# Performance work log

Hardware: AMD Instinct MI355X
Metric: run time of the kernel (lower is better)

Reference implementation:

```python
import jax, jax.numpy as jnp
import numpy as np
import math

B_, L_, E_, N_, K_, R_ = 2, 4096, 2048, 16, 4, 64


def setup_inputs() -> dict:
    key = jax.random.key(0)
    ks = jax.random.split(key, 8)
    x_inner = jax.random.normal(ks[0], (B_, L_, E_), jnp.float32)
    # depthwise conv params (weight squeezed to (E, K))
    conv_w = jax.random.normal(ks[1], (E_, K_), jnp.float32) * (1.0 / math.sqrt(K_))
    conv_b = jax.random.normal(ks[2], (E_,), jnp.float32) * 0.02
    # x_proj: Linear(E -> R + 2N), no bias; weight stored (out, in)
    x_proj_w = jax.random.normal(ks[3], (R_ + 2 * N_, E_), jnp.float32) * (E_ ** -0.5)
    # dt_proj: Linear(R -> E) with Mamba dt init
    dt_proj_w = jax.random.uniform(ks[4], (E_, R_), jnp.float32, -(E_ ** -0.5), E_ ** -0.5)
    dt = jnp.exp(jax.random.uniform(ks[5], (E_,), jnp.float32) * (math.log(0.1) - math.log(0.001)) + math.log(0.001))
    dt = jnp.clip(dt, 1e-4, None)
    dt_proj_b = dt + jnp.log(-jnp.expm1(-dt))  # inverse softplus
    # A_log: log of arange(1..N) tiled over channels; D = ones
    A_log = jnp.log(jnp.tile(jnp.arange(1, N_ + 1, dtype=jnp.float32), (E_, 1)))
    D = jnp.ones((E_,), jnp.float32)
    return {"x_inner": x_inner, "conv_w": conv_w, "conv_b": conv_b,
            "x_proj_w": x_proj_w, "dt_proj_w": dt_proj_w, "dt_proj_b": dt_proj_b,
            "A_log": A_log, "D": D}


def _forward(x_inner, conv_w, conv_b, x_proj_w, dt_proj_w, dt_proj_b, A_log, D):
    B, L, E = x_inner.shape
    N = A_log.shape[1]
    K = conv_w.shape[1]
    R = dt_proj_w.shape[1]
    # ---- causal depthwise conv1d + SiLU ----
    x_t = jnp.transpose(x_inner, (0, 2, 1))  # (B, E, L)
    x_t = jax.lax.conv_general_dilated(
        x_t, conv_w[:, None, :],  # (O=E, I=1, K)
        window_strides=(1,), padding=[(K - 1, 0)],
        feature_group_count=E,
        dimension_numbers=("NCH", "OIH", "NCH")) + conv_b[None, :, None]
    x_conv = jax.nn.silu(jnp.transpose(x_t, (0, 2, 1)))  # (B, L, E)
    # ---- input-dependent SSM parameters ----
    x_dbl = jnp.einsum("ble,oe->blo", x_conv, x_proj_w)  # (B, L, R+2N)
    dt_lowrank = x_dbl[..., :R]
    Bm = x_dbl[..., R:R + N]       # (B, L, N)
    Cm = x_dbl[..., R + N:]        # (B, L, N)
    delta = jax.nn.softplus(jnp.einsum("blr,er->ble", dt_lowrank, dt_proj_w) + dt_proj_b)  # (B, L, E)
    A = -jnp.exp(A_log)            # (E, N)
    # ---- selective scan over sequence ----
    def step(h, inp):
        d_t, b_t, c_t, u_t = inp   # (B,E), (B,N), (B,N), (B,E)
        dA = jnp.exp(d_t[..., None] * A)              # (B, E, N)
        h = dA * h + (d_t * u_t)[..., None] * b_t[:, None, :]
        y_t = jnp.einsum("ben,bn->be", h, c_t)
        return h, y_t

    h0 = jnp.zeros((B, E, N), x_conv.dtype)
    xs = (jnp.transpose(delta, (1, 0, 2)), jnp.transpose(Bm, (1, 0, 2)),
          jnp.transpose(Cm, (1, 0, 2)), jnp.transpose(x_conv, (1, 0, 2)))
    _, ys = jax.lax.scan(step, h0, xs)
    y = jnp.transpose(ys, (1, 0, 2)) + x_conv * D  # skip term D*u
    return y  # (B, L, E)


def reference(x_inner, conv_w, conv_b, x_proj_w, dt_proj_w, dt_proj_b, A_log, D):
    return _forward(x_inner, conv_w, conv_b, x_proj_w, dt_proj_w, dt_proj_b, A_log, D)
```

## Files before the change

### kernel.cpp

```cpp
#include <hip/hip_runtime.h>
#include <cstdint>
#include <cstddef>

#define BB 2
#define LL 4096
#define EE 2048
#define NN 16
#define RR 64
#define NCH 64
#define LC  64
#define BL  (BB*LL)
#define KS  16
#define STRIP 16

static constexpr size_t OFF_XCONV = 0;
static constexpr size_t OFF_DELTA = OFF_XCONV + (size_t)BB*LL*EE;
static constexpr size_t OFF_XDT   = OFF_DELTA + (size_t)BB*LL*EE;
static constexpr size_t OFF_P     = OFF_XDT   + (size_t)96*BL;
static constexpr size_t OFF_S     = OFF_P     + (size_t)NCH*BB*NN*EE;
static constexpr size_t OFF_H0    = OFF_S     + (size_t)NCH*BB*NN*EE;
static constexpr size_t OFF_BC    = OFF_H0    + (size_t)NCH*BB*NN*EE;
static constexpr size_t OFF_PART  = OFF_P;

#define L2E 1.4426950408889634f

__device__ __forceinline__ float fast_softplus(float z) {
  if (z > 20.f) return z;
  return 0.6931471805599453f * __log2f(1.f + __builtin_amdgcn_exp2f(z * L2E));
}

__global__ __launch_bounds__(256) void k_conv(const float* __restrict__ x,
    const float* __restrict__ cw, const float* __restrict__ cb,
    float* __restrict__ xc) {
  const int t     = threadIdx.x;
  const int eh    = blockIdx.x & 1;
  const int strip = (blockIdx.x >> 1) & (LL/STRIP - 1);
  const int b     = blockIdx.x >> 9;
  const int e0    = (eh*256 + t) * 4;
  const int l0    = strip * STRIP;
  const float4* cw4 = (const float4*)cw;
  const float4 w0 = cw4[e0 + 0], w1 = cw4[e0 + 1], w2 = cw4[e0 + 2], w3 = cw4[e0 + 3];
  const float b0 = cb[e0 + 0], b1 = cb[e0 + 1], b2 = cb[e0 + 2], b3 = cb[e0 + 3];
  const float* base = x + (size_t)b*LL*EE + e0;
  float* obase = xc + (size_t)b*LL*EE + e0;
  float4 win0, win1, win2;
  {
    const float4 z = make_float4(0.f, 0.f, 0.f, 0.f);
    win0 = (l0 - 3 >= 0) ? *(const float4*)(base + (size_t)(l0-3)*EE) : z;
    win1 = (l0 - 2 >= 0) ? *(const float4*)(base + (size_t)(l0-2)*EE) : z;
    win2 = (l0 - 1 >= 0) ? *(const float4*)(base + (size_t)(l0-1)*EE) : z;
  }
  #pragma unroll
  for (int i = 0; i < STRIP; ++i) {
    const int l = l0 + i;
    const float4 cur = *(const float4*)(base + (size_t)l*EE);
    float a0 = b0 + win0.x*w0.x + win1.x*w0.y + win2.x*w0.z + cur.x*w0.w;
    float a1 = b1 + win0.y*w1.x + win1.y*w1.y + win2.y*w1.z + cur.y*w1.w;
    float a2 = b2 + win0.z*w2.x + win1.z*w2.y + win2.z*w2.z + cur.z*w2.w;
    float a3 = b3 + win0.w*w3.x + win1.w*w3.y + win2.w*w3.z + cur.w*w3.w;
    a0 = a0 / (1.f + __builtin_amdgcn_exp2f(-a0 * L2E));
    a1 = a1 / (1.f + __builtin_amdgcn_exp2f(-a1 * L2E));
    a2 = a2 / (1.f + __builtin_amdgcn_exp2f(-a2 * L2E));
    a3 = a3 / (1.f + __builtin_amdgcn_exp2f(-a3 * L2E));
    float4 o; o.x = a0; o.y = a1; o.z = a2; o.w = a3;
    *(float4*)(obase + (size_t)l*EE) = o;
    win0 = win1; win1 = win2; win2 = cur;
  }
}

__global__ __launch_bounds__(256, 2) void k_xdbl(const float* __restrict__ xc,
    const float* __restrict__ xpw, float* __restrict__ part) {
  __shared__ float xs[128*36];
  __shared__ float wsh[96*34];
  const int t  = threadIdx.x;
  const int mt = blockIdx.x >> 4;
  const int ks = blockIdx.x & 15;
  const int row0  = mt * 128;
  const int kbase = ks * (EE/KS);
  const int tr = t & 15;
  const int tc = t >> 4;
  const int c0 = 6 * tc;
  float acc[8][6];
  #pragma unroll
  for (int i = 0; i < 8; ++i)
    #pragma unroll
    for (int j = 0; j < 6; ++j) acc[i][j] = 0.f;

  const int xr = t >> 3;
  const int xk = (t & 7) * 4;
  const int wo = t >> 5;
  const int wk = t & 31;

  for (int ch = 0; ch < (EE/KS)/32; ++ch) {
    const int koff = kbase + ch * 32;
    __syncthreads();
    #pragma unroll
    for (int p = 0; p < 4; ++p) {
      int r = xr + 32 * p;
      float4 v = *(const float4*)(xc + (size_t)(row0 + r)*EE + koff + xk);
      *(float4*)(xs + r*36 + xk) = v;
    }
    #pragma unroll
    for (int p = 0; p < 12; ++p) {
      int o = wo + 8 * p;
      wsh[o*34 + wk] = xpw[(size_t)o*EE + koff + wk];
    }
    __syncthreads();
    #pragma unroll
    for (int kk = 0; kk < 32; kk += 2) {
      float2 xf[8], wf[6];
      #pragma unroll
      for (int i = 0; i < 8; ++i) xf[i] = *(const float2*)(xs + (tr + 16*i)*36 + kk);
      #pragma unroll
      for (int j = 0; j < 6; ++j) wf[j] = *(const float2*)(wsh + (c0 + j)*34 + kk);
      #pragma unroll
      for (int i = 0; i < 8; ++i)
        #pragma unroll
        for (int j = 0; j < 6; ++j) {
          acc[i][j] += xf[i].x * wf[j].x;
          acc[i][j] += xf[i].y * wf[j].y;
        }
    }
  }
  #pragma unroll
  for (int i = 0; i < 8; ++i)
    #pragma unroll
    for (int j = 0; j < 6; ++j)
      part[((size_t)ks*96 + (c0 + j))*BL + row0 + tr + 16*i] = acc[i][j];
}

__global__ __launch_bounds__(256) void k_combine(const float* __restrict__ part,
    float* __restrict__ xdT) {
  int i = blockIdx.x * 256 + threadIdx.x;
  float4 s = ((const float4*)part)[i];
  #pragma unroll
  for (int ks = 1; ks < KS; ++ks) {
    float4 v = ((const float4*)part)[(size_t)ks*(96*BL/4) + i];
    s.x += v.x; s.y += v.y; s.z += v.z; s.w += v.w;
  }
  ((float4*)xdT)[i] = s;
}

__global__ __launch_bounds__(256) void k_pack(const float* __restrict__ xdT,
    float* __restrict__ BC) {
  __shared__ float tile[64][33];
  const int t = threadIdx.x;
  const int bl0 = blockIdx.x * 64;
  const int jr = t >> 6, bll = t & 63;
  #pragma unroll
  for (int p = 0; p < 8; ++p) {
    int j = jr + 4 * p;
    tile[bll][j] = xdT[(size_t)(64 + j)*BL + bl0 + bll];
  }
  __syncthreads();
  const int blw = t >> 3;
  const int j4 = (t & 7) * 4;
  #pragma unroll
  for (int p = 0; p < 2; ++p) {
    int bl = blw + 32 * p;
    float4 v = make_float4(tile[bl][j4], tile[bl][j4+1], tile[bl][j4+2], tile[bl][j4+3]);
    *(float4*)(BC + (size_t)(bl0 + bl)*32 + j4) = v;
  }
}

__global__ __launch_bounds__(256, 2) void k_delta(const float* __restrict__ xdT,
    const float* __restrict__ dtw, const float* __restrict__ dtb,
    float* __restrict__ dl) {
  __shared__ float xs[128*66];
  __shared__ float wsh[128*66];
  const int t  = threadIdx.x;
  const int rt = blockIdx.x >> 4;
  const int et = blockIdx.x & 15;
  const int row0 = rt * 128;
  const int eb   = et * 128;
  #pragma unroll
  for (int p = 0; p < 32; ++p) {
    int idx = t + 256*p;
    int k = idx >> 7, rr = idx & 127;
    xs[rr*66 + k] = xdT[(size_t)k*BL + row0 + rr];
  }
  #pragma unroll
  for (int p = 0; p < 32; ++p) {
    int idx = t + 256*p;
    int e = idx >> 6, k = idx & 63;
    wsh[e*66 + k] = dtw[(size_t)(eb + e)*RR + k];
  }
  __syncthreads();
  const int tr = t >> 4;
  const int tc = t & 15;
  float acc[8][8];
  #pragma unroll
  for (int i = 0; i < 8; ++i)
    #pragma unroll
    for (int j = 0; j < 8; ++j) acc[i][j] = 0.f;
  for (int k = 0; k < 64; k += 2) {
    float2 xf[8], wf[8];
    #pragma unroll
    for (int i = 0; i < 8; ++i) xf[i] = *(const float2*)(xs + (tr + 16*i)*66 + k);
    #pragma unroll
    for (int j = 0; j < 8; ++j) wf[j] = *(const float2*)(wsh + (tc + 16*j)*66 + k);
    #pragma unroll
    for (int i = 0; i < 8; ++i)
      #pragma unroll
      for (int j = 0; j < 8; ++j) {
        acc[i][j] += xf[i].x * wf[j].x;
        acc[i][j] += xf[i].y * wf[j].y;
      }
  }
  #pragma unroll
  for (int j = 0; j < 8; ++j) {
    int e = eb + tc + 16*j;
    float bias = dtb[e];
    #pragma unroll
    for (int i = 0; i < 8; ++i) {
      float z = acc[i][j] + bias;
      dl[(size_t)(row0 + tr + 16*i)*EE + e] = fast_softplus(z);
    }
  }
}

__global__ __launch_bounds__(256) void k_scanA(const float* __restrict__ dl,
    const float* __restrict__ xc, const float* __restrict__ BC,
    float* __restrict__ P, float* __restrict__ S) {
  const int t  = threadIdx.x;
  const int eb = (blockIdx.x & 7) << 8;
  const int b  = (blockIdx.x >> 3) & 1;
  const int c  = blockIdx.x >> 4;
  const int e  = eb + t;
  const int l0 = c * LC;
  float h[NN];
  #pragma unroll
  for (int n = 0; n < NN; ++n) h[n] = 0.f;
  const float* dp = dl + (size_t)(b*LL + l0)*EE + e;
  const float* up = xc + (size_t)(b*LL + l0)*EE + e;
  const float* bc = BC + (size_t)(b*LL + l0)*32;
  float dsum = 0.f;
  float d_nx = dp[0], u_nx = up[0];
  #pragma unroll 2
  for (int l = 0; l < LC; ++l) {
    float d = d_nx, u = u_nx;
    d_nx = dp[(size_t)(l+1)*EE];
    u_nx = up[(size_t)(l+1)*EE];
    float w = d * u;
    dsum += d;
    float q = __builtin_amdgcn_exp2f(-d * L2E);
    float pw[NN];
    pw[0]=q; pw[1]=q*q; pw[2]=pw[1]*q; pw[3]=pw[1]*pw[1];
    pw[4]=pw[3]*q; pw[5]=pw[3]*pw[1]; pw[6]=pw[3]*pw[2]; pw[7]=pw[3]*pw[3];
    #pragma unroll
    for (int n = 8; n < 16; ++n) pw[n] = pw[7]*pw[n-8];
    #pragma unroll
    for (int n = 0; n < NN; ++n)
      h[n] = pw[n]*h[n] + w*bc[l*32 + n];
  }
  float Q = __builtin_amdgcn_exp2f(-dsum * L2E);
  float Pq[NN];
  Pq[0]=Q; Pq[1]=Q*Q; Pq[2]=Pq[1]*Q; Pq[3]=Pq[1]*Pq[1];
  Pq[4]=Pq[3]*Q; Pq[5]=Pq[3]*Pq[1]; Pq[6]=Pq[3]*Pq[2]; Pq[7]=Pq[3]*Pq[3];
  #pragma unroll
  for (int n = 8; n < 16; ++n) Pq[n] = Pq[7]*Pq[n-8];
  const size_t base = (size_t)(c*BB + b)*NN*EE + e;
  #pragma unroll
  for (int n = 0; n < NN; ++n) { P[base + (size_t)n*EE] = Pq[n]; S[base + (size_t)n*EE] = h[n]; }
}

__global__ __launch_bounds__(256) void k_chain(const float* __restrict__ P,
    const float* __restrict__ S, float* __restrict__ h0) {
  int i = blockIdx.x * 256 + threadIdx.x;
  float h = 0.f;
  float Pc = P[i], Sc = S[i];
  for (int c = 0; c < NCH; ++c) {
    size_t idx = (size_t)c*(BB*NN*EE) + i;
    float Pn = 0.f, Sn = 0.f;
    if (c + 1 < NCH) {
      Pn = P[idx + (size_t)(BB*NN*EE)];
      Sn = S[idx + (size_t)(BB*NN*EE)];
    }
    h0[idx] = h;
    h = Pc*h + Sc;
    Pc = Pn; Sc = Sn;
  }
}

__global__ __launch_bounds__(256) void k_scanY(const float* __restrict__ dl,
    const float* __restrict__ xc, const float* __restrict__ BC,
    const float* __restrict__ h0, const float* __restrict__ Dp,
    float* __restrict__ out) {
  const int t  = threadIdx.x;
  const int eb = (blockIdx.x & 7) << 8;
  const int b  = (blockIdx.x >> 3) & 1;
  const int c  = blockIdx.x >> 4;
  const int e  = eb + t;
  const int l0 = c * LC;
  float h[NN];
  #pragma unroll
  for (int n = 0; n < NN; ++n)
    h[n] = h0[(size_t)c*(BB*NN*EE) + (size_t)b*(NN*EE) + (size_t)n*EE + e];
  const float Dv = Dp[e];
  const float* dp = dl + (size_t)(b*LL + l0)*EE + e;
  const float* up = xc + (size_t)(b*LL + l0)*EE + e;
  const float* bc = BC + (size_t)(b*LL + l0)*32;
  float* op = out + (size_t)(b*LL + l0)*EE + e;
  float d_nx = dp[0], u_nx = up[0];
  #pragma unroll 2
  for (int l = 0; l < LC; ++l) {
    float d = d_nx, u = u_nx;
    d_nx = dp[(size_t)(l+1)*EE];
    u_nx = up[(size_t)(l+1)*EE];
    float w = d * u;
    float q = __builtin_amdgcn_exp2f(-d * L2E);
    float pw[NN];
    pw[0]=q; pw[1]=q*q; pw[2]=pw[1]*q; pw[3]=pw[1]*pw[1];
    pw[4]=pw[3]*q; pw[5]=pw[3]*pw[1]; pw[6]=pw[3]*pw[2]; pw[7]=pw[3]*pw[3];
    #pragma unroll
    for (int n = 8; n < 16; ++n) pw[n] = pw[7]*pw[n-8];
    float y0 = 0.f, y1 = 0.f, y2 = 0.f, y3 = 0.f;
    #pragma unroll
    for (int n = 0; n < NN; ++n) {
      h[n] = pw[n]*h[n] + w*bc[l*32 + n];
      float hv = h[n] * bc[l*32 + 16 + n];
      if ((n & 3) == 0) y0 += hv; else if ((n & 3) == 1) y1 += hv;
      else if ((n & 3) == 2) y2 += hv; else y3 += hv;
    }
    op[(size_t)l*EE] = (y0 + y1) + (y2 + y3) + u*Dv;
  }
}

extern "C" void kernel_launch(void* const* d_in, const int* in_sizes, int n_in,
                              void* d_out, int out_size, void* d_ws, size_t ws_size,
                              hipStream_t stream) {
  const float* x    = (const float*)d_in[0];
  const float* cw   = (const float*)d_in[1];
  const float* cb   = (const float*)d_in[2];
  const float* xpw  = (const float*)d_in[3];
  const float* dtw  = (const float*)d_in[4];
  const float* dtb  = (const float*)d_in[5];
  const float* Dp   = (const float*)d_in[7];
  float* ws = (float*)d_ws;
  float* xconv = ws + OFF_XCONV;
  float* delta = ws + OFF_DELTA;
  float* xdT   = ws + OFF_XDT;
  float* part  = ws + OFF_PART;
  float* P     = ws + OFF_P;
  float* S     = ws + OFF_S;
  float* h0    = ws + OFF_H0;
  float* BC    = ws + OFF_BC;
  float* out   = (float*)d_out;

  k_conv   <<<BB*2*(LL/STRIP),    256, 0, stream>>>(x, cw, cb, xconv);
  k_xdbl   <<<64*KS,              256, 0, stream>>>(xconv, xpw, part);
  k_combine<<<(96*BL/4)/256,      256, 0, stream>>>(part, xdT);
  k_pack   <<<BL/64,              256, 0, stream>>>(xdT, BC);
  k_delta  <<<64*16,              256, 0, stream>>>(xdT, dtw, dtb, delta);
  k_scanA  <<<(EE/256)*BB*NCH,    256, 0, stream>>>(delta, xconv, BC, P, S);
  k_chain  <<<(BB*NN*EE)/256,     256, 0, stream>>>(P, S, h0);
  k_scanY  <<<(EE/256)*BB*NCH,    256, 0, stream>>>(delta, xconv, BC, h0, Dp, out);
}
```

Before: 330.0 us.

## Use split-bf16 MFMA for x_proj GEMM and store conv output as bf16 hi/lo

The x_proj GEMM moves from scalar FP32 FMAs to bf16 MFMA 16x16x32 instructions. Each FP32 value is split into a bf16 high part and a bf16 low residual, and three MFMAs per tile recover near-FP32 accuracy. The conv kernel now writes x_conv as two bf16 planes, and a new kernel converts the weights the same way. The scans rebuild u from both planes, and the K-split drops from 16 to 4, so the partial sums and the combine step shrink. The truncating conversion and the dropped lo*lo term cost some precision, and the scans do extra unpacking work.

```diff
diff --git a/kernel.cpp b/kernel.cpp
--- a/kernel.cpp
+++ b/kernel.cpp
@@ -10,49 +10,74 @@
 #define NCH 64
 #define LC  64
 #define BL  (BB*LL)
-#define KS  16
+#define KSX 4
+#define AKS (EE/KSX)
 #define STRIP 16
 
-static constexpr size_t OFF_XCONV = 0;
-static constexpr size_t OFF_DELTA = OFF_XCONV + (size_t)BB*LL*EE;
+static constexpr size_t OFF_XCH   = 0;
+static constexpr size_t OFF_XCL   = OFF_XCH + (size_t)BB*LL*EE/2;
+static constexpr size_t OFF_DELTA = OFF_XCL + (size_t)BB*LL*EE/2;
 static constexpr size_t OFF_XDT   = OFF_DELTA + (size_t)BB*LL*EE;
 static constexpr size_t OFF_P     = OFF_XDT   + (size_t)96*BL;
 static constexpr size_t OFF_S     = OFF_P     + (size_t)NCH*BB*NN*EE;
 static constexpr size_t OFF_H0    = OFF_S     + (size_t)NCH*BB*NN*EE;
 static constexpr size_t OFF_BC    = OFF_H0    + (size_t)NCH*BB*NN*EE;
 static constexpr size_t OFF_PART  = OFF_P;
+static constexpr size_t OFF_WHL   = OFF_S;
 
 #define L2E 1.4426950408889634f
+
+typedef __attribute__((ext_vector_type(8))) short short8;
+typedef __attribute__((ext_vector_type(4))) float f32x4;
 
 __device__ __forceinline__ float fast_softplus(float z) {
   if (z > 20.f) return z;
   return 0.6931471805599453f * __log2f(1.f + __builtin_amdgcn_exp2f(z * L2E));
 }
+__device__ __forceinline__ unsigned short f2bf(float x) {
+  union { float f; unsigned int i; } u; u.f = x; return (unsigned short)(u.i >> 16);
+}
+__device__ __forceinline__ float bf2f(unsigned short h) {
+  union { float f; unsigned int i; } u; u.i = (unsigned int)h << 16; return u.f;
+}
+
+__global__ __launch_bounds__(256) void k_wcvt(const float* __restrict__ xpw,
+    unsigned short* __restrict__ whl) {
+  const size_t i = ((size_t)blockIdx.x * 256 + threadIdx.x) * 4;
+  float4 v = *(const float4*)(xpw + i);
+  unsigned short h0 = f2bf(v.x), h1 = f2bf(v.y), h2 = f2bf(v.z), h3 = f2bf(v.w);
+  ushort4 vh = make_ushort4(h0, h1, h2, h3);
+  ushort4 vl = make_ushort4(f2bf(v.x - bf2f(h0)), f2bf(v.y - bf2f(h1)),
+                            f2bf(v.z - bf2f(h2)), f2bf(v.w - bf2f(h3)));
+  *(ushort4*)(whl + i) = vh;
+  *(ushort4*)(whl + (size_t)96*EE + i) = vl;
+}
 
 __global__ __launch_bounds__(256) void k_conv(const float* __restrict__ x,
     const float* __restrict__ cw, const float* __restrict__ cb,
-    float* __restrict__ xc) {
+    unsigned short* __restrict__ xch, unsigned short* __restrict__ xcl) {
   const int t     = threadIdx.x;
   const int eh    = blockIdx.x & 1;
   const int strip = (blockIdx.x >> 1) & (LL/STRIP - 1);
   const int b     = blockIdx.x >> 9;
   const int e0    = (eh*256 + t) * 4;
-  const int l0    = strip * STRIP;
+  const int lbase = strip * STRIP;
   const float4* cw4 = (const float4*)cw;
   const float4 w0 = cw4[e0 + 0], w1 = cw4[e0 + 1], w2 = cw4[e0 + 2], w3 = cw4[e0 + 3];
   const float b0 = cb[e0 + 0], b1 = cb[e0 + 1], b2 = cb[e0 + 2], b3 = cb[e0 + 3];
   const float* base = x + (size_t)b*LL*EE + e0;
-  float* obase = xc + (size_t)b*LL*EE + e0;
+  unsigned short* oh = xch + (size_t)b*LL*EE + e0;
+  unsigned short* ol = xcl + (size_t)b*LL*EE + e0;
   float4 win0, win1, win2;
   {
     const float4 z = make_float4(0.f, 0.f, 0.f, 0.f);
-    win0 = (l0 - 3 >= 0) ? *(const float4*)(base + (size_t)(l0-3)*EE) : z;
-    win1 = (l0 - 2 >= 0) ? *(const float4*)(base + (size_t)(l0-2)*EE) : z;
-    win2 = (l0 - 1 >= 0) ? *(const float4*)(base + (size_t)(l0-1)*EE) : z;
+    win0 = (lbase - 3 >= 0) ? *(const float4*)(base + (size_t)(lbase-3)*EE) : z;
+    win1 = (lbase - 2 >= 0) ? *(const float4*)(base + (size_t)(lbase-2)*EE) : z;
+    win2 = (lbase - 1 >= 0) ? *(const float4*)(base + (size_t)(lbase-1)*EE) : z;
   }
   #pragma unroll
   for (int i = 0; i < STRIP; ++i) {
-    const int l = l0 + i;
+    const int l = lbase + i;
     const float4 cur = *(const float4*)(base + (size_t)l*EE);
     float a0 = b0 + win0.x*w0.x + win1.x*w0.y + win2.x*w0.z + cur.x*w0.w;
     float a1 = b1 + win0.y*w1.x + win1.y*w1.y + win2.y*w1.z + cur.y*w1.w;
@@ -62,71 +87,104 @@
     a1 = a1 / (1.f + __builtin_amdgcn_exp2f(-a1 * L2E));
     a2 = a2 / (1.f + __builtin_amdgcn_exp2f(-a2 * L2E));
     a3 = a3 / (1.f + __builtin_amdgcn_exp2f(-a3 * L2E));
-    float4 o; o.x = a0; o.y = a1; o.z = a2; o.w = a3;
-    *(float4*)(obase + (size_t)l*EE) = o;
+    unsigned short h0 = f2bf(a0), h1 = f2bf(a1), h2 = f2bf(a2), h3 = f2bf(a3);
+    ushort4 vh = make_ushort4(h0, h1, h2, h3);
+    ushort4 vl = make_ushort4(f2bf(a0 - bf2f(h0)), f2bf(a1 - bf2f(h1)),
+                              f2bf(a2 - bf2f(h2)), f2bf(a3 - bf2f(h3)));
+    *(ushort4*)(oh + (size_t)l*EE) = vh;
+    *(ushort4*)(ol + (size_t)l*EE) = vl;
     win0 = win1; win1 = win2; win2 = cur;
   }
 }
 
-__global__ __launch_bounds__(256, 2) void k_xdbl(const float* __restrict__ xc,
-    const float* __restrict__ xpw, float* __restrict__ part) {
-  __shared__ float xs[128*36];
-  __shared__ float wsh[96*34];
-  const int t  = threadIdx.x;
-  const int mt = blockIdx.x >> 4;
-  const int ks = blockIdx.x & 15;
-  const int row0  = mt * 128;
-  const int kbase = ks * (EE/KS);
-  const int tr = t & 15;
-  const int tc = t >> 4;
-  const int c0 = 6 * tc;
-  float acc[8][6];
-  #pragma unroll
-  for (int i = 0; i < 8; ++i)
-    #pragma unroll
-    for (int j = 0; j < 6; ++j) acc[i][j] = 0.f;
-
-  const int xr = t >> 3;
-  const int xk = (t & 7) * 4;
-  const int wo = t >> 5;
-  const int wk = t & 31;
-
-  for (int ch = 0; ch < (EE/KS)/32; ++ch) {
-    const int koff = kbase + ch * 32;
+__global__ __launch_bounds__(256) void k_xdbl(const unsigned short* __restrict__ xch,
+    const unsigned short* __restrict__ xcl, const unsigned short* __restrict__ whl,
+    float* __restrict__ part) {
+  __shared__ unsigned short sm[12800];
+  unsigned short* Ah = sm;
+  unsigned short* Al = sm + 2560;
+  unsigned short* Bh = sm + 5120;
+  unsigned short* Bl = sm + 8960;
+  const unsigned short* wh = whl;
+  const unsigned short* wl = whl + (size_t)96*EE;
+
+  const int t   = threadIdx.x;
+  const int mt  = blockIdx.x >> 2;
+  const int ks  = blockIdx.x & 3;
+  const int row0 = mt * 64;
+  const int k0   = ks * AKS;
+
+  const int ar = t >> 2, aq = t & 3;
+  const int br = t >> 2, bq = t & 3;
+  const int br2 = 64 + (t >> 2);
+  const unsigned short* pAh = xch + (size_t)(row0 + ar)*EE + k0 + aq*8;
+  const unsigned short* pAl = xcl + (size_t)(row0 + ar)*EE + k0 + aq*8;
+  const unsigned short* pBh0 = wh + (size_t)br*EE + k0 + bq*8;
+  const unsigned short* pBl0 = wl + (size_t)br*EE + k0 + bq*8;
+  const unsigned short* pBh1 = wh + (size_t)br2*EE + k0 + bq*8;
+  const unsigned short* pBl1 = wl + (size_t)br2*EE + k0 + bq*8;
+
+  const int lane = t & 63, wv = t >> 6;
+  const int arow = wv*16 + (lane & 15);
+  const int kq   = (lane >> 4) * 8;
+  const int obase = (lane & 15)*40 + kq;
+
+  f32x4 acc[6];
+  #pragma unroll
+  for (int j = 0; j < 6; ++j) acc[j] = (f32x4){0.f, 0.f, 0.f, 0.f};
+
+  uint4 rah = *(const uint4*)(pAh);
+  uint4 ral = *(const uint4*)(pAl);
+  uint4 rbh0 = *(const uint4*)(pBh0);
+  uint4 rbl0 = *(const uint4*)(pBl0);
+  uint4 rbh1, rbl1;
+  if (t < 128) { rbh1 = *(const uint4*)(pBh1); rbl1 = *(const uint4*)(pBl1); }
+
+  for (int kt = 0; kt < AKS/32; ++kt) {
     __syncthreads();
-    #pragma unroll
-    for (int p = 0; p < 4; ++p) {
-      int r = xr + 32 * p;
-      float4 v = *(const float4*)(xc + (size_t)(row0 + r)*EE + koff + xk);
-      *(float4*)(xs + r*36 + xk) = v;
-    }
-    #pragma unroll
-    for (int p = 0; p < 12; ++p) {
-      int o = wo + 8 * p;
-      wsh[o*34 + wk] = xpw[(size_t)o*EE + koff + wk];
+    *(uint4*)(Ah + ar*40 + aq*8) = rah;
+    *(uint4*)(Al + ar*40 + aq*8) = ral;
+    *(uint4*)(Bh + br*40 + bq*8) = rbh0;
+    *(uint4*)(Bl + br*40 + bq*8) = rbl0;
+    if (t < 128) {
+      *(uint4*)(Bh + br2*40 + bq*8) = rbh1;
+      *(uint4*)(Bl + br2*40 + bq*8) = rbl1;
+    }
+    if (kt + 1 < AKS/32) {
+      const int ko = (kt + 1) * 32;
+      rah = *(const uint4*)(pAh + ko);
+      ral = *(const uint4*)(pAl + ko);
+      rbh0 = *(const uint4*)(pBh0 + ko);
+      rbl0 = *(const uint4*)(pBl0 + ko);
+      if (t < 128) { rbh1 = *(const uint4*)(pBh1 + ko); rbl1 = *(const uint4*)(pBl1 + ko); }
     }
     __syncthreads();
-    #pragma unroll
-    for (int kk = 0; kk < 32; kk += 2) {
-      float2 xf[8], wf[6];
-      #pragma unroll
-      for (int i = 0; i < 8; ++i) xf[i] = *(const float2*)(xs + (tr + 16*i)*36 + kk);
-      #pragma unroll
-      for (int j = 0; j < 6; ++j) wf[j] = *(const float2*)(wsh + (c0 + j)*34 + kk);
-      #pragma unroll
-      for (int i = 0; i < 8; ++i)
-        #pragma unroll
-        for (int j = 0; j < 6; ++j) {
-          acc[i][j] += xf[i].x * wf[j].x;
-          acc[i][j] += xf[i].y * wf[j].y;
-        }
-    }
-  }
-  #pragma unroll
-  for (int i = 0; i < 8; ++i)
-    #pragma unroll
-    for (int j = 0; j < 6; ++j)
-      part[((size_t)ks*96 + (c0 + j))*BL + row0 + tr + 16*i] = acc[i][j];
+    short8 ah = *(const short8*)(Ah + arow*40 + kq);
+    short8 al = *(const short8*)(Al + arow*40 + kq);
+    #pragma unroll
+    for (int j = 0; j < 6; ++j) {
+      short8 bh = *(const short8*)(Bh + j*640 + obase);
+      short8 bl = *(const short8*)(Bl + j*640 + obase);
+      acc[j] = __builtin_amdgcn_mfma_f32_16x16x32_bf16(ah, bh, acc[j], 0, 0, 0);
+      acc[j] = __builtin_amdgcn_mfma_f32_16x16x32_bf16(ah, bl, acc[j], 0, 0, 0);
+      acc[j] = __builtin_amdgcn_mfma_f32_16x16x32_bf16(al, bh, acc[j], 0, 0, 0);
+    }
+  }
+
+  __syncthreads();
+  float* tile = (float*)sm;
+  #pragma unroll
+  for (int j = 0; j < 6; ++j)
+    #pragma unroll
+    for (int i = 0; i < 4; ++i)
+      tile[(wv*16 + (lane >> 4)*4 + i)*97 + j*16 + (lane & 15)] = acc[j][i];
+  __syncthreads();
+  #pragma unroll
+  for (int p = 0; p < 24; ++p) {
+    int idx = p*256 + t;
+    int o = idx >> 6, r = idx & 63;
+    part[((size_t)ks*96 + o)*BL + row0 + r] = tile[r*97 + o];
+  }
 }
 
 __global__ __launch_bounds__(256) void k_combine(const float* __restrict__ part,
@@ -134,7 +192,7 @@
   int i = blockIdx.x * 256 + threadIdx.x;
   float4 s = ((const float4*)part)[i];
   #pragma unroll
-  for (int ks = 1; ks < KS; ++ks) {
+  for (int ks = 1; ks < KSX; ++ks) {
     float4 v = ((const float4*)part)[(size_t)ks*(96*BL/4) + i];
     s.x += v.x; s.y += v.y; s.z += v.z; s.w += v.w;
   }
@@ -220,7 +278,8 @@
 }
 
 __global__ __launch_bounds__(256) void k_scanA(const float* __restrict__ dl,
-    const float* __restrict__ xc, const float* __restrict__ BC,
+    const unsigned short* __restrict__ xch, const unsigned short* __restrict__ xcl,
+    const float* __restrict__ BC,
     float* __restrict__ P, float* __restrict__ S) {
   const int t  = threadIdx.x;
   const int eb = (blockIdx.x & 7) << 8;
@@ -232,15 +291,16 @@
   #pragma unroll
   for (int n = 0; n < NN; ++n) h[n] = 0.f;
   const float* dp = dl + (size_t)(b*LL + l0)*EE + e;
-  const float* up = xc + (size_t)(b*LL + l0)*EE + e;
+  const unsigned short* uh = xch + (size_t)(b*LL + l0)*EE + e;
+  const unsigned short* ul = xcl + (size_t)(b*LL + l0)*EE + e;
   const float* bc = BC + (size_t)(b*LL + l0)*32;
   float dsum = 0.f;
-  float d_nx = dp[0], u_nx = up[0];
+  float d_nx = dp[0], u_nx = bf2f(uh[0]) + bf2f(ul[0]);
   #pragma unroll 2
   for (int l = 0; l < LC; ++l) {
     float d = d_nx, u = u_nx;
     d_nx = dp[(size_t)(l+1)*EE];
-    u_nx = up[(size_t)(l+1)*EE];
+    u_nx = bf2f(uh[(size_t)(l+1)*EE]) + bf2f(ul[(size_t)(l+1)*EE]);
     float w = d * u;
     dsum += d;
     float q = __builtin_amdgcn_exp2f(-d * L2E);
@@ -283,7 +343,8 @@
 }
 
 __global__ __launch_bounds__(256) void k_scanY(const float* __restrict__ dl,
-    const float* __restrict__ xc, const float* __restrict__ BC,
+    const unsigned short* __restrict__ xch, const unsigned short* __restrict__ xcl,
+    const float* __restrict__ BC,
     const float* __restrict__ h0, const float* __restrict__ Dp,
     float* __restrict__ out) {
   const int t  = threadIdx.x;
@@ -298,15 +359,16 @@
     h[n] = h0[(size_t)c*(BB*NN*EE) + (size_t)b*(NN*EE) + (size_t)n*EE + e];
   const float Dv = Dp[e];
   const float* dp = dl + (size_t)(b*LL + l0)*EE + e;
-  const float* up = xc + (size_t)(b*LL + l0)*EE + e;
+  const unsigned short* uh = xch + (size_t)(b*LL + l0)*EE + e;
+  const unsigned short* ul = xcl + (size_t)(b*LL + l0)*EE + e;
   const float* bc = BC + (size_t)(b*LL + l0)*32;
   float* op = out + (size_t)(b*LL + l0)*EE + e;
-  float d_nx = dp[0], u_nx = up[0];
+  float d_nx = dp[0], u_nx = bf2f(uh[0]) + bf2f(ul[0]);
   #pragma unroll 2
   for (int l = 0; l < LC; ++l) {
     float d = d_nx, u = u_nx;
     d_nx = dp[(size_t)(l+1)*EE];
-    u_nx = up[(size_t)(l+1)*EE];
+    u_nx = bf2f(uh[(size_t)(l+1)*EE]) + bf2f(ul[(size_t)(l+1)*EE]);
     float w = d * u;
     float q = __builtin_amdgcn_exp2f(-d * L2E);
     float pw[NN];
@@ -337,7 +399,9 @@
   const float* dtb  = (const float*)d_in[5];
   const float* Dp   = (const float*)d_in[7];
   float* ws = (float*)d_ws;
-  float* xconv = ws + OFF_XCONV;
+  unsigned short* xch = (unsigned short*)(ws + OFF_XCH);
+  unsigned short* xcl = (unsigned short*)(ws + OFF_XCL);
+  unsigned short* whl = (unsigned short*)(ws + OFF_WHL);
   float* delta = ws + OFF_DELTA;
   float* xdT   = ws + OFF_XDT;
   float* part  = ws + OFF_PART;
@@ -347,12 +411,13 @@
   float* BC    = ws + OFF_BC;
   float* out   = (float*)d_out;
 
-  k_conv   <<<BB*2*(LL/STRIP),    256, 0, stream>>>(x, cw, cb, xconv);
-  k_xdbl   <<<64*KS,              256, 0, stream>>>(xconv, xpw, part);
+  k_wcvt   <<<(96*EE/4)/256,      256, 0, stream>>>(xpw, whl);
+  k_conv   <<<BB*2*(LL/STRIP),    256, 0, stream>>>(x, cw, cb, xch, xcl);
+  k_xdbl   <<<(BL/64)*KSX,        256, 0, stream>>>(xch, xcl, whl, part);
   k_combine<<<(96*BL/4)/256,      256, 0, stream>>>(part, xdT);
   k_pack   <<<BL/64,              256, 0, stream>>>(xdT, BC);
   k_delta  <<<64*16,              256, 0, stream>>>(xdT, dtw, dtb, delta);
-  k_scanA  <<<(EE/256)*BB*NCH,    256, 0, stream>>>(delta, xconv, BC, P, S);
+  k_scanA  <<<(EE/256)*BB*NCH,    256, 0, stream>>>(delta, xch, xcl, BC, P, S);
   k_chain  <<<(BB*NN*EE)/256,     256, 0, stream>>>(P, S, h0);
-  k_scanY  <<<(EE/256)*BB*NCH,    256, 0, stream>>>(delta, xconv, BC, h0, Dp, out);
-}
+  k_scanY  <<<(EE/256)*BB*NCH,    256, 0, stream>>>(delta, xch, xcl, BC, h0, Dp, out);
+}
```

New measurement: 292.3 us. 1.13x faster.
